# Optimization experiments

Hardware: AMD Instinct MI355X
Metric: run time of the kernel (lower is better)

Reference implementation:

```python
import jax, jax.numpy as jnp
import numpy as np

N_NODES = 40000
N_EDGES = 640000
D = 128
N_LAYERS = 3


def setup_inputs() -> dict:
    key = jax.random.key(0)
    ks = jax.random.split(key, 6)
    x = jax.random.normal(ks[0], (N_NODES, D), dtype=jnp.float32)
    src = jax.random.randint(ks[1], (N_EDGES,), 0, N_NODES, dtype=jnp.int32)
    dst = jax.random.randint(ks[2], (N_EDGES,), 0, N_NODES, dtype=jnp.int32)
    scale = 1.0 / np.sqrt(D)
    w_self = jax.random.normal(ks[3], (N_LAYERS, D, D), dtype=jnp.float32) * scale
    w_neigh = jax.random.normal(ks[4], (N_LAYERS, D, D), dtype=jnp.float32) * scale
    b = jax.random.normal(ks[5], (N_LAYERS, D), dtype=jnp.float32) * scale
    return {"x": x, "src": src, "dst": dst, "w_self": w_self, "w_neigh": w_neigh, "b": b}


def reference(x, src, dst, w_self, w_neigh, b):
    # in-degree per destination node (clamped to avoid div-by-zero, matching mean aggregator)
    deg = jax.ops.segment_sum(jnp.ones_like(dst, dtype=x.dtype), dst, num_segments=N_NODES)
    inv_deg = (1.0 / jnp.maximum(deg, 1.0))[:, None]  # [N,1]

    h = x
    for l in range(N_LAYERS):
        # mean aggregation over in-neighbors: gather src feats, scatter-add to dst
        agg = jax.ops.segment_sum(h[src], dst, num_segments=N_NODES) * inv_deg  # [N,D]
        h = h @ w_self[l] + agg @ w_neigh[l] + b[l]  # SAGEConv: fc_self + fc_neigh + bias
        if l < N_LAYERS - 1:
            h = jax.nn.relu(h)  # dropout p=0.0 -> identity
    return h
```

## Files before the change

### kernel.cpp

```cpp
#include <hip/hip_runtime.h>

#define N_NODES 40000
#define N_EDGES 640000
#define DIM 128
#define N_LAYERS 3
#define STRIDE 64

typedef _Float16 half_t;
typedef __attribute__((ext_vector_type(8))) _Float16 f16x8_t;
typedef __attribute__((ext_vector_type(4))) float f32x4_t;

__global__ void scatterprep_kernel(const int* __restrict__ src, const int* __restrict__ dst,
                                   int* __restrict__ cnt, int* __restrict__ pcsr,
                                   const float* __restrict__ x, half_t* __restrict__ h,
                                   const float* __restrict__ w_self, const float* __restrict__ w_neigh,
                                   half_t* __restrict__ wt) {
    const int SB = (N_EDGES + 255) / 256;
    if (blockIdx.x < SB) {
        int i = blockIdx.x * 256 + threadIdx.x;
        if (i < N_EDGES) {
            int d = dst[i];
            int pos = atomicAdd(&cnt[d], 1);
            if (pos < STRIDE) pcsr[d * STRIDE + pos] = src[i];
        }
        return;
    }
    int i = (blockIdx.x - SB) * 256 + threadIdx.x;
    const int NS = N_NODES * DIM / 8;
    if (i < NS) {
        const float4* p = (const float4*)x + (size_t)i * 2;
        float4 a = p[0], b = p[1];
        f16x8_t v;
        v[0] = (half_t)a.x; v[1] = (half_t)a.y; v[2] = (half_t)a.z; v[3] = (half_t)a.w;
        v[4] = (half_t)b.x; v[5] = (half_t)b.y; v[6] = (half_t)b.z; v[7] = (half_t)b.w;
        *(f16x8_t*)&h[(size_t)i * 8] = v;
    } else {
        int j = i - NS;
        if (j < N_LAYERS * 2 * DIM * DIM) {
            int k = j & (DIM - 1);
            int n = (j >> 7) & (DIM - 1);
            int ls = j >> 14;
            int l = ls >> 1, s = ls & 1;
            const float* W = (s ? w_neigh : w_self) + (size_t)l * DIM * DIM;
            wt[j] = (half_t)W[k * DIM + n];
        }
    }
}

__global__ void agg_kernel(const half_t* __restrict__ h,
                           const int* __restrict__ cnt,
                           const int* __restrict__ pcsr,
                           half_t* __restrict__ agg) {
    int node = (blockIdx.x * blockDim.x + threadIdx.x) >> 6;
    int lane = threadIdx.x & 63;
    if (node >= N_NODES) return;
    const int g = lane >> 4, c = lane & 15;
    int deg = cnt[node];
    int nd = deg < STRIDE ? deg : STRIDE;
    int e0 = node * STRIDE, e1 = e0 + nd;
    float acc[8] = {0.f, 0.f, 0.f, 0.f, 0.f, 0.f, 0.f, 0.f};
    for (int base = e0; base < e1; base += 16) {
        float f[4];
        f16x8_t v[4];
#pragma unroll
        for (int s = 0; s < 4; ++s) {
            int ee = base + 4 * s + g;
            bool ok = ee < e1;
            f[s] = ok ? 1.f : 0.f;
            int sidx = ok ? pcsr[ee] : 0;
            v[s] = *(const f16x8_t*)&h[(size_t)sidx * DIM + c * 8];
        }
#pragma unroll
        for (int s = 0; s < 4; ++s)
#pragma unroll
            for (int j = 0; j < 8; ++j)
                acc[j] = fmaf(f[s], (float)v[s][j], acc[j]);
    }
#pragma unroll
    for (int j = 0; j < 8; ++j) {
        acc[j] += __shfl_xor(acc[j], 16, 64);
        acc[j] += __shfl_xor(acc[j], 32, 64);
    }
    if (g == 0) {
        float w = 1.0f / fmaxf((float)deg, 1.0f);
        f16x8_t o;
#pragma unroll
        for (int j = 0; j < 8; ++j) o[j] = (half_t)(acc[j] * w);
        *(f16x8_t*)&agg[(size_t)node * DIM + c * 8] = o;
    }
}

#define LDSN 136
__global__ __launch_bounds__(256) void gemm_kernel(
    half_t* __restrict__ h, const half_t* __restrict__ agg,
    const half_t* __restrict__ wt,
    const float* __restrict__ bias, float* __restrict__ fout,
    int write_f32, int relu) {
    __shared__ half_t sW[2 * DIM][LDSN];
    const int tid = threadIdx.x;
    const int wave = tid >> 6, lane = tid & 63;
    const int quad = lane >> 4, m = lane & 15;
    const int rowW = blockIdx.x * 128 + wave * 32;

#pragma unroll
    for (int c4 = 0; c4 < 16; ++c4) {
        int c = (c4 << 8) + tid;
        int part = c & 15;
        int n = c >> 4;
        *(f16x8_t*)&sW[n][part * 8] = *(const f16x8_t*)&wt[(size_t)n * DIM + part * 8];
    }
    __syncthreads();

    f32x4_t acc[2][8];
#pragma unroll
    for (int a = 0; a < 2; ++a)
#pragma unroll
        for (int b = 0; b < 8; ++b) acc[a][b] = {0.f, 0.f, 0.f, 0.f};

#pragma unroll
    for (int s = 0; s < 2; ++s) {
        const half_t* A = s ? agg : h;
        const int nb = s * DIM;
#pragma unroll
        for (int k2 = 0; k2 < 4; ++k2) {
            const int kg = (k2 << 5) + quad * 8;
            f16x8_t B[8];
#pragma unroll
            for (int jt = 0; jt < 8; ++jt)
                B[jt] = *(const f16x8_t*)&sW[nb + jt * 16 + m][kg];
#pragma unroll
            for (int rt = 0; rt < 2; ++rt) {
                int r = rowW + rt * 16 + m;
                r = (r < N_NODES) ? r : (N_NODES - 1);
                f16x8_t a = *(const f16x8_t*)&A[(size_t)r * DIM + kg];
#pragma unroll
                for (int jt = 0; jt < 8; ++jt)
                    acc[rt][jt] = __builtin_amdgcn_mfma_f32_16x16x32_f16(a, B[jt], acc[rt][jt], 0, 0, 0);
            }
        }
    }

#pragma unroll
    for (int rt = 0; rt < 2; ++rt)
#pragma unroll
        for (int jt = 0; jt < 8; ++jt) {
            int col = jt * 16 + m;
            float bv = bias[col];
#pragma unroll
            for (int r4 = 0; r4 < 4; ++r4) {
                int row = rowW + rt * 16 + quad * 4 + r4;
                if (row >= N_NODES) continue;
                float v = acc[rt][jt][r4] + bv;
                if (relu) v = fmaxf(v, 0.f);
                if (write_f32) {
                    fout[(size_t)row * DIM + col] = v;
                } else {
                    h[(size_t)row * DIM + col] = (half_t)v;
                }
            }
        }
}


extern "C" void kernel_launch(void* const* d_in, const int* in_sizes, int n_in,
                              void* d_out, int out_size, void* d_ws, size_t ws_size,
                              hipStream_t stream) {
    const float* x      = (const float*)d_in[0];
    const int*   src    = (const int*)d_in[1];
    const int*   dst    = (const int*)d_in[2];
    const float* w_self = (const float*)d_in[3];
    const float* w_neigh= (const float*)d_in[4];
    const float* b      = (const float*)d_in[5];
    float* out = (float*)d_out;

    char* ws = (char*)d_ws;
    half_t* h    = (half_t*)ws; ws += (size_t)N_NODES * DIM * 2;
    half_t* agg  = (half_t*)ws; ws += (size_t)N_NODES * DIM * 2;
    half_t* wt   = (half_t*)ws; ws += (size_t)N_LAYERS * 2 * DIM * DIM * 2;
    int*   cnt   = (int*)ws;    ws += (size_t)N_NODES * 4;
    int*   pcsr  = (int*)ws;    ws += (size_t)N_NODES * STRIDE * 4;

    hipMemsetAsync(cnt, 0, (size_t)N_NODES * 4, stream);

    const int SB = (N_EDGES + 255) / 256;
    const int PREP_ITEMS = N_NODES * DIM / 8 + N_LAYERS * 2 * DIM * DIM;
    const int PB = (PREP_ITEMS + 255) / 256;
    scatterprep_kernel<<<SB + PB, 256, 0, stream>>>(src, dst, cnt, pcsr,
                                                    x, h, w_self, w_neigh, wt);

    const int GEMM_BLOCKS = (N_NODES + 127) / 128;
    for (int l = 0; l < N_LAYERS; ++l) {
        agg_kernel<<<(N_NODES * 64 + 255) / 256, 256, 0, stream>>>(h, cnt, pcsr, agg);
        int last = (l == N_LAYERS - 1);
        gemm_kernel<<<GEMM_BLOCKS, 256, 0, stream>>>(
            h, agg, wt + (size_t)l * 2 * DIM * DIM, b + (size_t)l * DIM,
            out, last ? 1 : 0, last ? 0 : 1);
    }
}
```

Measured before the change: 232.8 us.

## Quantize node features to int8 with per-row scales for gather aggregation

```diff
diff --git a/kernel.cpp b/kernel.cpp
--- a/kernel.cpp
+++ b/kernel.cpp
@@ -11,8 +11,9 @@
 typedef __attribute__((ext_vector_type(4))) float f32x4_t;
 
 __global__ void scatterprep_kernel(const int* __restrict__ src, const int* __restrict__ dst,
-                                   int* __restrict__ cnt, int* __restrict__ pcsr,
+                                   int* __restrict__ cnt, unsigned short* __restrict__ pcsr,
                                    const float* __restrict__ x, half_t* __restrict__ h,
+                                   unsigned char* __restrict__ hq, float* __restrict__ hsc,
                                    const float* __restrict__ w_self, const float* __restrict__ w_neigh,
                                    half_t* __restrict__ wt) {
     const int SB = (N_EDGES + 255) / 256;
@@ -21,7 +22,7 @@
         if (i < N_EDGES) {
             int d = dst[i];
             int pos = atomicAdd(&cnt[d], 1);
-            if (pos < STRIDE) pcsr[d * STRIDE + pos] = src[i];
+            if (pos < STRIDE) pcsr[d * STRIDE + pos] = (unsigned short)src[i];
         }
         return;
     }
@@ -29,11 +30,36 @@
     const int NS = N_NODES * DIM / 8;
     if (i < NS) {
         const float4* p = (const float4*)x + (size_t)i * 2;
-        float4 a = p[0], b = p[1];
-        f16x8_t v;
-        v[0] = (half_t)a.x; v[1] = (half_t)a.y; v[2] = (half_t)a.z; v[3] = (half_t)a.w;
-        v[4] = (half_t)b.x; v[5] = (half_t)b.y; v[6] = (half_t)b.z; v[7] = (half_t)b.w;
-        *(f16x8_t*)&h[(size_t)i * 8] = v;
+        float4 a = p[0], b2 = p[1];
+        float v[8] = {a.x, a.y, a.z, a.w, b2.x, b2.y, b2.z, b2.w};
+        f16x8_t hv;
+        float mx = 0.f;
+#pragma unroll
+        for (int j = 0; j < 8; ++j) {
+            hv[j] = (half_t)v[j];
+            mx = fmaxf(mx, fabsf((float)hv[j]));
+        }
+        *(f16x8_t*)&h[(size_t)i * 8] = hv;
+        mx = fmaxf(mx, __shfl_xor(mx, 1));
+        mx = fmaxf(mx, __shfl_xor(mx, 2));
+        mx = fmaxf(mx, __shfl_xor(mx, 4));
+        mx = fmaxf(mx, __shfl_xor(mx, 8));
+        mx = fmaxf(mx, 1e-20f);
+        float inv = 127.f / mx;
+        unsigned int lo = 0, hi = 0;
+#pragma unroll
+        for (int j = 0; j < 4; ++j) {
+            int q = (int)rintf((float)hv[j] * inv) + 128;
+            lo |= ((unsigned int)q) << (8 * j);
+        }
+#pragma unroll
+        for (int j = 0; j < 4; ++j) {
+            int q = (int)rintf((float)hv[4 + j] * inv) + 128;
+            hi |= ((unsigned int)q) << (8 * j);
+        }
+        uint2 pk; pk.x = lo; pk.y = hi;
+        *(uint2*)&hq[(size_t)i * 8] = pk;
+        if ((i & 15) == 0) hsc[i >> 4] = mx / 127.f;
     } else {
         int j = i - NS;
         if (j < N_LAYERS * 2 * DIM * DIM) {
@@ -47,9 +73,8 @@
     }
 }
 
-__global__ void agg_kernel(const half_t* __restrict__ h,
-                           const int* __restrict__ cnt,
-                           const int* __restrict__ pcsr,
+__global__ void agg_kernel(const unsigned char* __restrict__ hq, const float* __restrict__ hsc,
+                           const int* __restrict__ cnt, const unsigned short* __restrict__ pcsr,
                            half_t* __restrict__ agg) {
     int node = (blockIdx.x * blockDim.x + threadIdx.x) >> 6;
     int lane = threadIdx.x & 63;
@@ -59,23 +84,32 @@
     int nd = deg < STRIDE ? deg : STRIDE;
     int e0 = node * STRIDE, e1 = e0 + nd;
     float acc[8] = {0.f, 0.f, 0.f, 0.f, 0.f, 0.f, 0.f, 0.f};
+    float ssum = 0.f;
     for (int base = e0; base < e1; base += 16) {
-        float f[4];
-        f16x8_t v[4];
+        float sf[4];
+        uint2 q[4];
 #pragma unroll
         for (int s = 0; s < 4; ++s) {
             int ee = base + 4 * s + g;
             bool ok = ee < e1;
-            f[s] = ok ? 1.f : 0.f;
-            int sidx = ok ? pcsr[ee] : 0;
-            v[s] = *(const f16x8_t*)&h[(size_t)sidx * DIM + c * 8];
-        }
-#pragma unroll
-        for (int s = 0; s < 4; ++s)
-#pragma unroll
-            for (int j = 0; j < 8; ++j)
-                acc[j] = fmaf(f[s], (float)v[s][j], acc[j]);
-    }
+            int sidx = ok ? (int)pcsr[ee] : 0;
+            sf[s] = ok ? hsc[sidx] : 0.f;
+            q[s] = *(const uint2*)&hq[(size_t)sidx * DIM + c * 8];
+        }
+#pragma unroll
+        for (int s = 0; s < 4; ++s) {
+            ssum += sf[s];
+            unsigned int lo = q[s].x, hi = q[s].y;
+#pragma unroll
+            for (int j = 0; j < 4; ++j)
+                acc[j] = fmaf(sf[s], (float)((lo >> (8 * j)) & 0xFF), acc[j]);
+#pragma unroll
+            for (int j = 0; j < 4; ++j)
+                acc[4 + j] = fmaf(sf[s], (float)((hi >> (8 * j)) & 0xFF), acc[4 + j]);
+        }
+    }
+#pragma unroll
+    for (int j = 0; j < 8; ++j) acc[j] -= 128.f * ssum;
 #pragma unroll
     for (int j = 0; j < 8; ++j) {
         acc[j] += __shfl_xor(acc[j], 16, 64);
@@ -91,12 +125,15 @@
 }
 
 #define LDSN 136
+#define SCRP 132
 __global__ __launch_bounds__(256) void gemm_kernel(
     half_t* __restrict__ h, const half_t* __restrict__ agg,
     const half_t* __restrict__ wt,
     const float* __restrict__ bias, float* __restrict__ fout,
+    unsigned char* __restrict__ hq, float* __restrict__ hsc,
     int write_f32, int relu) {
     __shared__ half_t sW[2 * DIM][LDSN];
+    half_t (*sScr)[SCRP] = (half_t(*)[SCRP])sW;
     const int tid = threadIdx.x;
     const int wave = tid >> 6, lane = tid & 63;
     const int quad = lane >> 4, m = lane & 15;
@@ -140,6 +177,8 @@
         }
     }
 
+    __syncthreads();
+
 #pragma unroll
     for (int rt = 0; rt < 2; ++rt)
 #pragma unroll
@@ -148,17 +187,52 @@
             float bv = bias[col];
 #pragma unroll
             for (int r4 = 0; r4 < 4; ++r4) {
-                int row = rowW + rt * 16 + quad * 4 + r4;
+                int rloc = wave * 32 + rt * 16 + quad * 4 + r4;
+                int row = blockIdx.x * 128 + rloc;
                 if (row >= N_NODES) continue;
                 float v = acc[rt][jt][r4] + bv;
                 if (relu) v = fmaxf(v, 0.f);
                 if (write_f32) {
                     fout[(size_t)row * DIM + col] = v;
                 } else {
-                    h[(size_t)row * DIM + col] = (half_t)v;
+                    half_t hv = (half_t)v;
+                    h[(size_t)row * DIM + col] = hv;
+                    sScr[rloc][col] = hv;
                 }
             }
         }
+
+    if (!write_f32) {
+        __syncthreads();
+        int rl = tid >> 1, hf = tid & 1;
+        int row = blockIdx.x * 128 + rl;
+        if (row < N_NODES) {
+            float mx = 0.f;
+#pragma unroll
+            for (int k8 = 0; k8 < 8; ++k8) {
+                f16x8_t vv = *(const f16x8_t*)&sScr[rl][hf * 64 + k8 * 8];
+#pragma unroll
+                for (int j = 0; j < 8; ++j) mx = fmaxf(mx, fabsf((float)vv[j]));
+            }
+            mx = fmaxf(mx, __shfl_xor(mx, 1));
+            mx = fmaxf(mx, 1e-20f);
+            float inv = 127.f / mx;
+#pragma unroll
+            for (int k8 = 0; k8 < 8; ++k8) {
+                f16x8_t vv = *(const f16x8_t*)&sScr[rl][hf * 64 + k8 * 8];
+                unsigned int lo = 0, hi = 0;
+#pragma unroll
+                for (int j = 0; j < 4; ++j)
+                    lo |= ((unsigned int)((int)rintf((float)vv[j] * inv) + 128)) << (8 * j);
+#pragma unroll
+                for (int j = 0; j < 4; ++j)
+                    hi |= ((unsigned int)((int)rintf((float)vv[4 + j] * inv) + 128)) << (8 * j);
+                uint2 pk; pk.x = lo; pk.y = hi;
+                *(uint2*)&hq[(size_t)row * DIM + hf * 64 + k8 * 8] = pk;
+            }
+            if (hf == 0) hsc[row] = mx / 127.f;
+        }
+    }
 }
 
 
@@ -174,11 +248,13 @@
     float* out = (float*)d_out;
 
     char* ws = (char*)d_ws;
-    half_t* h    = (half_t*)ws; ws += (size_t)N_NODES * DIM * 2;
-    half_t* agg  = (half_t*)ws; ws += (size_t)N_NODES * DIM * 2;
-    half_t* wt   = (half_t*)ws; ws += (size_t)N_LAYERS * 2 * DIM * DIM * 2;
-    int*   cnt   = (int*)ws;    ws += (size_t)N_NODES * 4;
-    int*   pcsr  = (int*)ws;    ws += (size_t)N_NODES * STRIDE * 4;
+    half_t* h    = (half_t*)ws;         ws += (size_t)N_NODES * DIM * 2;
+    half_t* agg  = (half_t*)ws;         ws += (size_t)N_NODES * DIM * 2;
+    half_t* wt   = (half_t*)ws;         ws += (size_t)N_LAYERS * 2 * DIM * DIM * 2;
+    unsigned char* hq = (unsigned char*)ws; ws += (size_t)N_NODES * DIM;
+    float* hsc   = (float*)ws;          ws += (size_t)N_NODES * 4;
+    int*   cnt   = (int*)ws;            ws += (size_t)N_NODES * 4;
+    unsigned short* pcsr = (unsigned short*)ws; ws += (size_t)N_NODES * STRIDE * 2;
 
     hipMemsetAsync(cnt, 0, (size_t)N_NODES * 4, stream);
 
@@ -186,14 +262,14 @@
     const int PREP_ITEMS = N_NODES * DIM / 8 + N_LAYERS * 2 * DIM * DIM;
     const int PB = (PREP_ITEMS + 255) / 256;
     scatterprep_kernel<<<SB + PB, 256, 0, stream>>>(src, dst, cnt, pcsr,
-                                                    x, h, w_self, w_neigh, wt);
+                                                    x, h, hq, hsc, w_self, w_neigh, wt);
 
     const int GEMM_BLOCKS = (N_NODES + 127) / 128;
     for (int l = 0; l < N_LAYERS; ++l) {
-        agg_kernel<<<(N_NODES * 64 + 255) / 256, 256, 0, stream>>>(h, cnt, pcsr, agg);
+        agg_kernel<<<(N_NODES * 64 + 255) / 256, 256, 0, stream>>>(hq, hsc, cnt, pcsr, agg);
         int last = (l == N_LAYERS - 1);
         gemm_kernel<<<GEMM_BLOCKS, 256, 0, stream>>>(
             h, agg, wt + (size_t)l * 2 * DIM * DIM, b + (size_t)l * DIM,
-            out, last ? 1 : 0, last ? 0 : 1);
-    }
-}
+            out, hq, hsc, last ? 1 : 0, last ? 0 : 1);
+    }
+}
```

Result: no change. 234.8 us (+0.8%).
